# Kernel optimization log

Measured on AMD Instinct MI355X. Metric: run time of the kernel, lower is better.

## Reference

```python
import jax, jax.numpy as jnp
import numpy as np

N_NODES = 100000
N_EDGES = 1600000
IN_FEATS = 128
NUM_HEADS = 4
OUT_FEATS = 32
NEG_SLOPE = 0.2


def setup_inputs() -> dict:
    key = jax.random.key(0)
    k1, k2, k3, k4, k5, k6 = jax.random.split(key, 6)
    feat = jax.random.normal(k1, (N_NODES, IN_FEATS), dtype=jnp.float32)
    src = jax.random.randint(k2, (N_EDGES,), 0, N_NODES, dtype=jnp.int32)
    dst = jnp.sort(jax.random.randint(k3, (N_EDGES,), 0, N_NODES, dtype=jnp.int32))
    # glorot-style scale ~ VarianceScaling(sqrt(2), fan_avg)
    w_scale = np.sqrt(2.0 * 2.0 / (IN_FEATS + NUM_HEADS * OUT_FEATS)).astype(np.float32)
    a_scale = np.sqrt(2.0 * 2.0 / (1 + OUT_FEATS)).astype(np.float32)
    W = jax.random.normal(k4, (IN_FEATS, NUM_HEADS * OUT_FEATS), dtype=jnp.float32) * w_scale
    attn_l = jax.random.normal(k5, (NUM_HEADS, OUT_FEATS), dtype=jnp.float32) * a_scale
    attn_r = jax.random.normal(k6, (NUM_HEADS, OUT_FEATS), dtype=jnp.float32) * a_scale
    return {"feat": feat, "src": src, "dst": dst, "W": W, "attn_l": attn_l, "attn_r": attn_r}


def reference(feat, src, dst, W, attn_l, attn_r):
    # Linear projection: [N, H, D]
    ft = (feat @ W).reshape(-1, NUM_HEADS, OUT_FEATS)
    # Per-node attention halves: [N, H]
    el = jnp.einsum("nhd,hd->nh", ft, attn_l)
    er = jnp.einsum("nhd,hd->nh", ft, attn_r)
    # Edge scores: e_ij = LeakyReLU(el[src] + er[dst])  -> [E, H]
    e = el[src] + er[dst]
    e = jnp.where(e > 0, e, NEG_SLOPE * e)
    # edge_softmax: per-destination segment softmax over incoming edges
    emax = jax.ops.segment_max(e, dst, num_segments=N_NODES)  # [N, H]
    ex = jnp.exp(e - emax[dst])                               # [E, H]
    esum = jax.ops.segment_sum(ex, dst, num_segments=N_NODES)  # [N, H]
    a = ex / esum[dst]                                         # [E, H]
    # Weighted scatter-sum aggregation: sum_j a_ij * W h_j -> [N, H, D]
    m = ft[src] * a[:, :, None]
    out = jax.ops.segment_sum(m, dst, num_segments=N_NODES)
    return out
```

## Files before the change

### kernel.cpp

```cpp
#include <hip/hip_runtime.h>

#define N_NODES 100000
#define N_EDGES 1600000
#define NUM_HEADS 4
#define NEG_SLOPE 0.2f
#define LDSTRIDE 136
#define CSTRIDE 132
#define SEG_BLOCKS 6250

typedef __attribute__((ext_vector_type(8))) short bf16x8;
typedef __attribute__((ext_vector_type(4))) float f32x4;

__device__ __forceinline__ unsigned short f2bf(float x) {
    union { float f; unsigned u; } v; v.f = x;
    unsigned r = v.u + 0x7fffu + ((v.u >> 16) & 1u);
    return (unsigned short)(r >> 16);
}
__device__ __forceinline__ float bflo(unsigned v) { return __uint_as_float(v << 16); }
__device__ __forceinline__ float bfhi(unsigned v) { return __uint_as_float(v & 0xffff0000u); }

__global__ __launch_bounds__(256) void prep_seg_kernel(
    const int* __restrict__ dst, int* __restrict__ seg,
    const float* __restrict__ W, unsigned short* __restrict__ Wt)
{
    const int b = blockIdx.x;
    if (b < SEG_BLOCKS) {
        int i = b * 256 + threadIdx.x;
        if (i >= N_EDGES) return;
        int d = dst[i];
        int dp = (i == 0) ? -1 : dst[i - 1];
        for (int n = dp + 1; n <= d; ++n) seg[n] = i;
        if (i == N_EDGES - 1)
            for (int n = d + 1; n <= N_NODES; ++n) seg[n] = N_EDGES;
    } else {
        int idx = (b - SEG_BLOCKS) * 256 + threadIdx.x;
        int n = idx >> 7, i = idx & 127;
        Wt[idx] = f2bf(W[i * 128 + n]);
    }
}

__global__ __launch_bounds__(256) void gemm_kernel(
    const float* __restrict__ feat, const unsigned short* __restrict__ Wt,
    const float* __restrict__ attn_l, const float* __restrict__ attn_r,
    unsigned short* __restrict__ ft, float* __restrict__ el,
    float* __restrict__ er)
{
    __shared__ __align__(16) unsigned short B_lds[128 * LDSTRIDE];
    __shared__ __align__(16) unsigned short A_lds[64 * LDSTRIDE];
    const int t = threadIdx.x;
    const int nbase = blockIdx.x * 64;

    {
        const int4* Wt4 = (const int4*)Wt;
#pragma unroll
        for (int i = 0; i < 8; ++i) {
            int idx = t + 256 * i;
            int n = idx >> 4, cg = idx & 15;
            *(int4*)(&B_lds[n * LDSTRIDE + cg * 8]) = Wt4[idx];
        }
    }
    {
        const float4* f4 = (const float4*)feat;
#pragma unroll
        for (int i = 0; i < 8; ++i) {
            int idx = t + 256 * i;
            int node = idx >> 5, kg = idx & 31;
            int g = nbase + node; if (g >= N_NODES) g = N_NODES - 1;
            float4 f = f4[g * 32 + kg];
            ushort4 u;
            u.x = f2bf(f.x); u.y = f2bf(f.y); u.z = f2bf(f.z); u.w = f2bf(f.w);
            *(ushort4*)(&A_lds[node * LDSTRIDE + kg * 4]) = u;
        }
    }
    __syncthreads();

    const int w = t >> 6, lane = t & 63;
    const int l15 = lane & 15, quad = lane >> 4;

    f32x4 acc[8];
#pragma unroll
    for (int c = 0; c < 8; ++c) acc[c] = (f32x4){0.f, 0.f, 0.f, 0.f};

    const unsigned short* Arow = &A_lds[(w * 16 + l15) * LDSTRIDE + quad * 8];
    const unsigned short* Brow = &B_lds[l15 * LDSTRIDE + quad * 8];
#pragma unroll
    for (int ks = 0; ks < 4; ++ks) {
        bf16x8 a = *(const bf16x8*)(Arow + ks * 32);
#pragma unroll
        for (int c = 0; c < 8; ++c) {
            bf16x8 b = *(const bf16x8*)(Brow + (c * 16) * LDSTRIDE + ks * 32);
            acc[c] = __builtin_amdgcn_mfma_f32_16x16x32_bf16(a, b, acc[c], 0, 0, 0);
        }
    }
    __syncthreads();

    float* C = (float*)B_lds;
#pragma unroll
    for (int c = 0; c < 8; ++c) {
#pragma unroll
        for (int reg = 0; reg < 4; ++reg) {
            C[(w * 16 + quad * 4 + reg) * CSTRIDE + c * 16 + l15] = acc[c][reg];
        }
    }
    __syncthreads();

    {
        const int row = t >> 2, q = t & 3;
        const int g = nbase + row;
        const float4* Crow = (const float4*)(C + row * CSTRIDE + q * 32);
        const float4* al = (const float4*)(attn_l + q * 32);
        const float4* ar = (const float4*)(attn_r + q * 32);
        float sl = 0.f, sr = 0.f;
        union { unsigned short u[32]; int4 v[4]; } pk;
#pragma unroll
        for (int i = 0; i < 8; ++i) {
            float4 f = Crow[i], a = al[i], b = ar[i];
            sl += f.x * a.x + f.y * a.y + f.z * a.z + f.w * a.w;
            sr += f.x * b.x + f.y * b.y + f.z * b.z + f.w * b.w;
            pk.u[4 * i + 0] = f2bf(f.x); pk.u[4 * i + 1] = f2bf(f.y);
            pk.u[4 * i + 2] = f2bf(f.z); pk.u[4 * i + 3] = f2bf(f.w);
        }
        if (g < N_NODES) {
#pragma unroll
            for (int k = 0; k < 4; ++k)
                *(int4*)(ft + (size_t)g * 128 + q * 32 + k * 8) = pk.v[k];
            el[g * 4 + q] = sl;
            er[g * 4 + q] = sr;
        }
    }
}

__global__ __launch_bounds__(256) void aggregate_kernel(
    const unsigned short* __restrict__ ft, const float* __restrict__ el,
    const float* __restrict__ er, const int* __restrict__ src,
    const int* __restrict__ seg, float* __restrict__ out)
{
    const int node = blockIdx.x * 4 + (threadIdx.x >> 6);
    if (node >= N_NODES) return;
    const int lane = threadIdx.x & 63;
    const int h4 = lane & 3;
    const int q4 = lane >> 2;
    const int qt = lane >> 4;
    const int l15 = lane & 15;
    const int hf = l15 >> 2;

    const int beg = __builtin_amdgcn_readfirstlane(seg[node]);
    const int end = __builtin_amdgcn_readfirstlane(seg[node + 1]);
    const float er_h = er[node * 4 + h4];

    float dpart = 0.f;
    float4 accA = make_float4(0.f, 0.f, 0.f, 0.f);
    float4 accB = make_float4(0.f, 0.f, 0.f, 0.f);

    for (int c0 = beg; c0 < end; c0 += 16) {
        const int L = end - c0;
        int cidx = c0 + q4; if (cidx >= end) cidx = end - 1;
        const int s = src[cidx];
        float e = el[s * 4 + h4] + er_h;
        e = (e > 0.f) ? e : NEG_SLOPE * e;
        const float p = (q4 < L) ? __expf(e) : 0.f;
        dpart += p;

        int sj[4];
#pragma unroll
        for (int k = 0; k < 4; ++k) sj[k] = __shfl(s, 16 * k + 4 * qt);
        int4 v[4];
#pragma unroll
        for (int k = 0; k < 4; ++k)
            v[k] = *(const int4*)(ft + (((size_t)(unsigned)sj[k]) << 7) + l15 * 8);
#pragma unroll
        for (int k = 0; k < 4; ++k) {
            const float pj = __shfl(p, 16 * k + 4 * qt + hf);
            accA.x += pj * bflo(v[k].x); accA.y += pj * bfhi(v[k].x);
            accA.z += pj * bflo(v[k].y); accA.w += pj * bfhi(v[k].y);
            accB.x += pj * bflo(v[k].z); accB.y += pj * bfhi(v[k].z);
            accB.z += pj * bflo(v[k].w); accB.w += pj * bfhi(v[k].w);
        }
    }

    dpart += __shfl_xor(dpart, 4);
    dpart += __shfl_xor(dpart, 8);
    dpart += __shfl_xor(dpart, 16);
    dpart += __shfl_xor(dpart, 32);
    accA.x += __shfl_xor(accA.x, 16); accA.y += __shfl_xor(accA.y, 16);
    accA.z += __shfl_xor(accA.z, 16); accA.w += __shfl_xor(accA.w, 16);
    accB.x += __shfl_xor(accB.x, 16); accB.y += __shfl_xor(accB.y, 16);
    accB.z += __shfl_xor(accB.z, 16); accB.w += __shfl_xor(accB.w, 16);
    accA.x += __shfl_xor(accA.x, 32); accA.y += __shfl_xor(accA.y, 32);
    accA.z += __shfl_xor(accA.z, 32); accA.w += __shfl_xor(accA.w, 32);
    accB.x += __shfl_xor(accB.x, 32); accB.y += __shfl_xor(accB.y, 32);
    accB.z += __shfl_xor(accB.z, 32); accB.w += __shfl_xor(accB.w, 32);

    const float dh = __shfl(dpart, hf);
    const float inv = (dh > 0.f) ? 1.f / dh : 0.f;

    if (qt == 0) {
        float4 o0 = make_float4(accA.x * inv, accA.y * inv, accA.z * inv, accA.w * inv);
        float4 o1 = make_float4(accB.x * inv, accB.y * inv, accB.z * inv, accB.w * inv);
        float* op = out + (size_t)node * 128 + l15 * 8;
        *(float4*)op = o0;
        *(float4*)(op + 4) = o1;
    }
}

extern "C" void kernel_launch(void* const* d_in, const int* in_sizes, int n_in,
                              void* d_out, int out_size, void* d_ws, size_t ws_size,
                              hipStream_t stream) {
    const float* feat   = (const float*)d_in[0];
    const int*   src    = (const int*)d_in[1];
    const int*   dst    = (const int*)d_in[2];
    const float* W      = (const float*)d_in[3];
    const float* attn_l = (const float*)d_in[4];
    const float* attn_r = (const float*)d_in[5];
    float* out = (float*)d_out;

    unsigned short* ft = (unsigned short*)d_ws;
    float* el  = (float*)(ft + (size_t)12800000);
    float* er  = el + 400000;
    unsigned short* Wt = (unsigned short*)(er + 400000);
    int* seg = (int*)(Wt + 16384);

    prep_seg_kernel<<<SEG_BLOCKS + 64, 256, 0, stream>>>(dst, seg, W, Wt);
    gemm_kernel<<<(N_NODES + 63) / 64, 256, 0, stream>>>(
        feat, Wt, attn_l, attn_r, ft, el, er);
    aggregate_kernel<<<(N_NODES + 3) / 4, 256, 0, stream>>>(
        ft, el, er, src, seg, out);
}
```

Measured before the change: 199.7 us.

## Fold attention vectors into weight matrix and write bf16 ft via LDS

Precomputes W·attn_l and W·attn_r as eight extra weight columns, so el/er come out of one extra MFMA per k-step rather than a separate fp32 epilogue dot product. The epilogue now packs accumulators to bf16 straight into the A tile in LDS and stores ft with coalesced int4 writes. That drops one barrier and the fp32 C staging buffer. The segment-boundary pass also handles four dst entries per thread with int4 loads. el/er now use bf16-rounded folded weights, which slightly changes their precision.

```diff
diff --git a/kernel.cpp b/kernel.cpp
--- a/kernel.cpp
+++ b/kernel.cpp
@@ -5,8 +5,7 @@
 #define NUM_HEADS 4
 #define NEG_SLOPE 0.2f
 #define LDSTRIDE 136
-#define CSTRIDE 132
-#define SEG_BLOCKS 6250
+#define SEG_BLOCKS 1563
 
 typedef __attribute__((ext_vector_type(8))) short bf16x8;
 typedef __attribute__((ext_vector_type(4))) float f32x4;
@@ -21,42 +20,59 @@
 
 __global__ __launch_bounds__(256) void prep_seg_kernel(
     const int* __restrict__ dst, int* __restrict__ seg,
-    const float* __restrict__ W, unsigned short* __restrict__ Wt)
+    const float* __restrict__ W, const float* __restrict__ attn_l,
+    const float* __restrict__ attn_r, unsigned short* __restrict__ Wt2)
 {
     const int b = blockIdx.x;
     if (b < SEG_BLOCKS) {
-        int i = b * 256 + threadIdx.x;
-        if (i >= N_EDGES) return;
-        int d = dst[i];
-        int dp = (i == 0) ? -1 : dst[i - 1];
-        for (int n = dp + 1; n <= d; ++n) seg[n] = i;
-        if (i == N_EDGES - 1)
-            for (int n = d + 1; n <= N_NODES; ++n) seg[n] = N_EDGES;
+        int i4 = b * 256 + threadIdx.x;
+        if (i4 >= N_EDGES / 4) return;
+        const int e0 = 4 * i4;
+        const int4 d = ((const int4*)dst)[i4];
+        const int dp = (e0 == 0) ? -1 : dst[e0 - 1];
+        for (int n = dp + 1; n <= d.x; ++n) seg[n] = e0;
+        for (int n = d.x + 1; n <= d.y; ++n) seg[n] = e0 + 1;
+        for (int n = d.y + 1; n <= d.z; ++n) seg[n] = e0 + 2;
+        for (int n = d.z + 1; n <= d.w; ++n) seg[n] = e0 + 3;
+        if (e0 + 4 == N_EDGES)
+            for (int n = d.w + 1; n <= N_NODES; ++n) seg[n] = N_EDGES;
     } else {
         int idx = (b - SEG_BLOCKS) * 256 + threadIdx.x;
-        int n = idx >> 7, i = idx & 127;
-        Wt[idx] = f2bf(W[i * 128 + n]);
+        if (idx >= 136 * 128) return;
+        int n = idx >> 7, k = idx & 127;
+        if (n < 128) {
+            Wt2[idx] = f2bf(W[k * 128 + n]);
+        } else {
+            int h = (n - 128) & 3;
+            const float* av = ((n - 128) < 4 ? attn_l : attn_r) + h * 32;
+            const float* col = W + k * 128 + h * 32;
+            float s = 0.f;
+#pragma unroll
+            for (int d2 = 0; d2 < 32; ++d2) s += col[d2] * av[d2];
+            Wt2[idx] = f2bf(s);
+        }
     }
 }
 
 __global__ __launch_bounds__(256) void gemm_kernel(
-    const float* __restrict__ feat, const unsigned short* __restrict__ Wt,
-    const float* __restrict__ attn_l, const float* __restrict__ attn_r,
+    const float* __restrict__ feat, const unsigned short* __restrict__ Wt2,
     unsigned short* __restrict__ ft, float* __restrict__ el,
     float* __restrict__ er)
 {
-    __shared__ __align__(16) unsigned short B_lds[128 * LDSTRIDE];
+    __shared__ __align__(16) unsigned short B_lds[136 * LDSTRIDE];
     __shared__ __align__(16) unsigned short A_lds[64 * LDSTRIDE];
     const int t = threadIdx.x;
     const int nbase = blockIdx.x * 64;
 
     {
-        const int4* Wt4 = (const int4*)Wt;
-#pragma unroll
-        for (int i = 0; i < 8; ++i) {
+        const int4* Wt4 = (const int4*)Wt2;
+#pragma unroll
+        for (int i = 0; i < 9; ++i) {
             int idx = t + 256 * i;
-            int n = idx >> 4, cg = idx & 15;
-            *(int4*)(&B_lds[n * LDSTRIDE + cg * 8]) = Wt4[idx];
+            if (idx < 2176) {
+                int n = idx >> 4, cg = idx & 15;
+                *(int4*)(&B_lds[n * LDSTRIDE + cg * 8]) = Wt4[idx];
+            }
         }
     }
     {
@@ -77,12 +93,13 @@
     const int w = t >> 6, lane = t & 63;
     const int l15 = lane & 15, quad = lane >> 4;
 
-    f32x4 acc[8];
-#pragma unroll
-    for (int c = 0; c < 8; ++c) acc[c] = (f32x4){0.f, 0.f, 0.f, 0.f};
+    f32x4 acc[9];
+#pragma unroll
+    for (int c = 0; c < 9; ++c) acc[c] = (f32x4){0.f, 0.f, 0.f, 0.f};
 
     const unsigned short* Arow = &A_lds[(w * 16 + l15) * LDSTRIDE + quad * 8];
     const unsigned short* Brow = &B_lds[l15 * LDSTRIDE + quad * 8];
+    const unsigned short* Brow8 = &B_lds[(128 + (l15 & 7)) * LDSTRIDE + quad * 8];
 #pragma unroll
     for (int ks = 0; ks < 4; ++ks) {
         bf16x8 a = *(const bf16x8*)(Arow + ks * 32);
@@ -91,41 +108,37 @@
             bf16x8 b = *(const bf16x8*)(Brow + (c * 16) * LDSTRIDE + ks * 32);
             acc[c] = __builtin_amdgcn_mfma_f32_16x16x32_bf16(a, b, acc[c], 0, 0, 0);
         }
+        bf16x8 b8 = *(const bf16x8*)(Brow8 + ks * 32);
+        acc[8] = __builtin_amdgcn_mfma_f32_16x16x32_bf16(a, b8, acc[8], 0, 0, 0);
+    }
+
+#pragma unroll
+    for (int reg = 0; reg < 4; ++reg) {
+        const int g = nbase + w * 16 + quad * 4 + reg;
+        if (g < N_NODES) {
+            if (l15 < 4)      el[g * 4 + l15] = acc[8][reg];
+            else if (l15 < 8) er[g * 4 + (l15 - 4)] = acc[8][reg];
+        }
+    }
+
+#pragma unroll
+    for (int c = 0; c < 8; ++c) {
+#pragma unroll
+        for (int reg = 0; reg < 4; ++reg) {
+            A_lds[(w * 16 + quad * 4 + reg) * LDSTRIDE + c * 16 + l15] =
+                f2bf(acc[c][reg]);
+        }
     }
     __syncthreads();
 
-    float* C = (float*)B_lds;
-#pragma unroll
-    for (int c = 0; c < 8; ++c) {
-#pragma unroll
-        for (int reg = 0; reg < 4; ++reg) {
-            C[(w * 16 + quad * 4 + reg) * CSTRIDE + c * 16 + l15] = acc[c][reg];
-        }
-    }
-    __syncthreads();
-
-    {
-        const int row = t >> 2, q = t & 3;
-        const int g = nbase + row;
-        const float4* Crow = (const float4*)(C + row * CSTRIDE + q * 32);
-        const float4* al = (const float4*)(attn_l + q * 32);
-        const float4* ar = (const float4*)(attn_r + q * 32);
-        float sl = 0.f, sr = 0.f;
-        union { unsigned short u[32]; int4 v[4]; } pk;
-#pragma unroll
-        for (int i = 0; i < 8; ++i) {
-            float4 f = Crow[i], a = al[i], b = ar[i];
-            sl += f.x * a.x + f.y * a.y + f.z * a.z + f.w * a.w;
-            sr += f.x * b.x + f.y * b.y + f.z * b.z + f.w * b.w;
-            pk.u[4 * i + 0] = f2bf(f.x); pk.u[4 * i + 1] = f2bf(f.y);
-            pk.u[4 * i + 2] = f2bf(f.z); pk.u[4 * i + 3] = f2bf(f.w);
-        }
+#pragma unroll
+    for (int i = 0; i < 4; ++i) {
+        int idx = t + 256 * i;
+        int node = idx >> 4, cg = idx & 15;
+        int g = nbase + node;
         if (g < N_NODES) {
-#pragma unroll
-            for (int k = 0; k < 4; ++k)
-                *(int4*)(ft + (size_t)g * 128 + q * 32 + k * 8) = pk.v[k];
-            el[g * 4 + q] = sl;
-            er[g * 4 + q] = sr;
+            int4 val = *(const int4*)(&A_lds[node * LDSTRIDE + cg * 8]);
+            *(int4*)(&ft[(size_t)g * 128 + cg * 8]) = val;
         }
     }
 }
@@ -217,12 +230,12 @@
     unsigned short* ft = (unsigned short*)d_ws;
     float* el  = (float*)(ft + (size_t)12800000);
     float* er  = el + 400000;
-    unsigned short* Wt = (unsigned short*)(er + 400000);
-    int* seg = (int*)(Wt + 16384);
-
-    prep_seg_kernel<<<SEG_BLOCKS + 64, 256, 0, stream>>>(dst, seg, W, Wt);
-    gemm_kernel<<<(N_NODES + 63) / 64, 256, 0, stream>>>(
-        feat, Wt, attn_l, attn_r, ft, el, er);
+    unsigned short* Wt2 = (unsigned short*)(er + 400000);
+    int* seg = (int*)(Wt2 + 136 * 128);
+
+    prep_seg_kernel<<<SEG_BLOCKS + 68, 256, 0, stream>>>(
+        dst, seg, W, attn_l, attn_r, Wt2);
+    gemm_kernel<<<(N_NODES + 63) / 64, 256, 0, stream>>>(feat, Wt2, ft, el, er);
     aggregate_kernel<<<(N_NODES + 3) / 4, 256, 0, stream>>>(
         ft, el, er, src, seg, out);
 }
```

Result: faster. 190.6 us (-4.6%).
